# Optimization experiments

Hardware: AMD Instinct MI355X
Metric: run time of the kernel (lower is better)

Reference implementation:

```python
import jax, jax.numpy as jnp
import numpy as np

B, C, L = 64, 128, 1024
SCALES = [8, 4, 2, 1]
EPS_BN = 1e-5


def _ema_vec(x_ds, alpha):
    # x_ds: [B, C, Ls]; alpha: [1, C, 1] in (0,1)
    Ls = x_ds.shape[-1]
    powers = jnp.arange(Ls - 1, -1, -1, dtype=x_ds.dtype)
    base = jnp.power(1.0 - alpha, powers)                                 # [1, C, Ls]
    w_num = jnp.concatenate([base[..., :1], base[..., 1:] * alpha], axis=-1)
    num = jnp.cumsum(x_ds * w_num, axis=-1)
    den = jnp.maximum(jnp.cumsum(base, axis=-1), 1e-12)
    return num / den


def _dwconv(x, w, s):
    # depthwise Conv1d: kernel 2s, stride s, pad s//2, groups=C, no bias
    return jax.lax.conv_general_dilated(
        x, w, window_strides=(s,), padding=[(s // 2, s // 2)],
        dimension_numbers=("NCH", "OIH", "NCH"), feature_group_count=C)


def _proj(v, w1, b1, w2, b2):
    # v: [B, C, Ls] -> Linear(Ls->L), exact GELU, Linear(L->L); torch Linear y = x @ W.T + b
    h = jax.nn.gelu(jnp.einsum("bcs,ls->bcl", v, w1) + b1, approximate=False)
    return jnp.einsum("bcl,ml->bcm", h, w2) + b2


def _hasd(x, bn_g, bn_b, branch, gate):
    Bn = x.shape[0]
    # BatchNorm1d over flattened (C*L) features, training-mode batch stats (biased var)
    v = x.reshape(Bn, C * L)
    mu = v.mean(axis=0)
    var = jnp.mean((v - mu) ** 2, axis=0)
    xn = (((v - mu) / jnp.sqrt(var + EPS_BN)) * bn_g + bn_b).reshape(Bn, C, L)
    trends, seasons, gates = [], [], []
    for s in SCALES:
        if s > 1:
            cw, w1, b1, w2, b2 = branch[s]
            down = _dwconv(xn, cw, s)                                     # [B, C, L//s]
            up = _proj(down, w1, b1, w2, b2)                              # [B, C, L]
        else:
            down = xn
            up = xn
        gw, gb, al = gate[s]
        alpha = jax.nn.sigmoid(al)
        trend_ds = _ema_vec(down, alpha)
        trend_up = _proj(trend_ds, w1, b1, w2, b2) if s > 1 else trend_ds
        season = up - trend_up
        trends.append(trend_up)
        seasons.append(season)
        gates.append(jax.nn.sigmoid(season.mean(axis=-1) @ gw.T + gb))    # [B, 1]
    g = jnp.concatenate(gates, axis=1)                                    # [B, n_scales]
    g = g / (g.sum(axis=1, keepdims=True) + 1e-6)
    g = g[:, :, None, None]
    trend_out = (jnp.stack(trends, axis=1) * g).sum(axis=1)
    season_out = (jnp.stack(seasons, axis=1) * g).sum(axis=1)
    return season_out, trend_out


def setup_inputs() -> dict:
    key = jax.random.key(0)
    ks = iter(jax.random.split(key, 64))
    d = {"x": jax.random.normal(next(ks), (B, C, L), jnp.float32)}
    d["bn_g"] = 1.0 + 0.1 * jax.random.normal(next(ks), (C * L,), jnp.float32)
    d["bn_b"] = 0.1 * jax.random.normal(next(ks), (C * L,), jnp.float32)
    for s in (8, 4, 2):
        Ls = L // s
        d[f"cw{s}"] = jax.random.normal(next(ks), (C, 1, 2 * s), jnp.float32) / np.sqrt(2 * s)
        d[f"w1_{s}"] = jax.random.normal(next(ks), (L, Ls), jnp.float32) / np.sqrt(Ls)
        d[f"b1_{s}"] = jnp.zeros((L,), jnp.float32)
        d[f"w2_{s}"] = jax.random.normal(next(ks), (L, L), jnp.float32) / np.sqrt(L)
        d[f"b2_{s}"] = jnp.zeros((L,), jnp.float32)
    for s in SCALES:
        d[f"gw{s}"] = jax.random.normal(next(ks), (1, C), jnp.float32) / np.sqrt(C)
        d[f"gb{s}"] = jnp.zeros((1,), jnp.float32)
        d[f"al{s}"] = jnp.full((1, C, 1), 0.3, jnp.float32)
    return d


def reference(x, bn_g, bn_b,
              cw8, w1_8, b1_8, w2_8, b2_8,
              cw4, w1_4, b1_4, w2_4, b2_4,
              cw2, w1_2, b1_2, w2_2, b2_2,
              gw8, gb8, al8, gw4, gb4, al4, gw2, gb2, al2, gw1, gb1, al1):
    branch = {8: (cw8, w1_8, b1_8, w2_8, b2_8),
              4: (cw4, w1_4, b1_4, w2_4, b2_4),
              2: (cw2, w1_2, b1_2, w2_2, b2_2)}
    gate = {8: (gw8, gb8, al8), 4: (gw4, gb4, al4),
            2: (gw2, gb2, al2), 1: (gw1, gb1, al1)}
    return _hasd(x, bn_g, bn_b, branch, gate)
```

## Files before the change

kernel.cpp:

```cpp
#include <hip/hip_runtime.h>
#include <hip/hip_bf16.h>
#include <math.h>

#define Bdim 64
#define Cdim 128
#define Ldim 1024
#define BC   (Bdim * Cdim)
#define CLn  (Cdim * Ldim)
#define TOT  (Bdim * CLn)

typedef unsigned short ushort_t;
typedef short s16x8 __attribute__((ext_vector_type(8)));
typedef float f32x4 __attribute__((ext_vector_type(4)));

__device__ __forceinline__ float bf2f(ushort_t u) {
    return __uint_as_float(((unsigned)u) << 16);
}
__device__ __forceinline__ ushort_t f2bf(float f) {
    __hip_bfloat16 h = __float2bfloat16(f);
    return *(ushort_t*)&h;
}
__device__ __forceinline__ void async16(const ushort_t* g, ushort_t* l) {
    __builtin_amdgcn_global_load_lds(
        (const __attribute__((address_space(1))) unsigned int*)g,
        (__attribute__((address_space(3))) unsigned int*)l, 16, 0, 0);
}
__device__ __forceinline__ float fast_gelu(float z) {
    float z2 = z * z;
    float inner = fmaf(0.044715f * z2, z, z);
    float e = __expf(-1.5957691216057308f * inner);
    return z * __builtin_amdgcn_rcpf(1.f + e);
}

__global__ __launch_bounds__(256) void bn_stats_kernel(
    const float* __restrict__ x, const float* __restrict__ bn_g,
    const float* __restrict__ bn_b, float* __restrict__ scale,
    float* __restrict__ shift)
{
    int f = blockIdx.x * 256 + threadIdx.x;
    float sum = 0.f, sumsq = 0.f;
    for (int b = 0; b < Bdim; ++b) {
        float v = x[(size_t)b * CLn + f];
        sum += v; sumsq += v * v;
    }
    float mu  = sum * (1.f / Bdim);
    float var = fmaxf(sumsq * (1.f / Bdim) - mu * mu, 0.f);
    float sc  = bn_g[f] / sqrtf(var + 1e-5f);
    scale[f] = sc;
    shift[f] = bn_b[f] - mu * sc;
}

__global__ __launch_bounds__(256) void convert_weights_kernel(
    const float* __restrict__ w1_8, const float* __restrict__ w1_4,
    const float* __restrict__ w1_2, const float* __restrict__ w2_8,
    const float* __restrict__ w2_4, const float* __restrict__ w2_2,
    ushort_t* __restrict__ dst)
{
    int idx = blockIdx.x * 256 + threadIdx.x;
    const float* src; int off;
    if      (idx < 131072)  { src = w1_8; off = 0; }
    else if (idx < 393216)  { src = w1_4; off = 131072; }
    else if (idx < 917504)  { src = w1_2; off = 393216; }
    else if (idx < 1966080) { src = w2_8; off = 917504; }
    else if (idx < 3014656) { src = w2_4; off = 1966080; }
    else                    { src = w2_2; off = 3014656; }
    dst[idx] = f2bf(src[idx - off]);
}

__global__ __launch_bounds__(256) void w2colsum_kernel(
    const float* __restrict__ w2_8, const float* __restrict__ w2_4,
    const float* __restrict__ w2_2, float* __restrict__ w2cs)
{
    const float* w = (blockIdx.y == 0) ? w2_8 : (blockIdx.y == 1) ? w2_4 : w2_2;
    int h  = blockIdx.x * 64 + (threadIdx.x & 63);
    int ls = threadIdx.x >> 6;
    float s = 0.f;
    for (int l = ls; l < 1024; l += 4) s += w[(size_t)l * 1024 + h];
    __shared__ float red[4][64];
    red[ls][threadIdx.x & 63] = s;
    __syncthreads();
    if (ls == 0)
        w2cs[blockIdx.y * 1024 + h] =
            red[0][threadIdx.x] + red[1][threadIdx.x] +
            red[2][threadIdx.x] + red[3][threadIdx.x];
}

__global__ __launch_bounds__(256) void ema_coef_kernel(
    const float* __restrict__ al1, const float* __restrict__ al2,
    const float* __restrict__ al4, const float* __restrict__ al8,
    float* __restrict__ coef, float* __restrict__ am)
{
    int c   = blockIdx.x;
    int tid = threadIdx.x;
    const float* als[4] = {al1, al2, al4, al8};
    const int Lss[4]    = {1024, 512, 256, 128};
    const int offs[4]   = {0, 1024, 1536, 1792};
#pragma unroll
    for (int si = 0; si < 4; ++si) {
        double a  = 1.0 / (1.0 + exp(-(double)als[si][c]));
        double m  = 1.0 - a;
        double lm = log(m);
        int Ls = Lss[si];
        for (int t = tid; t < Ls; t += 256) {
            double dt  = (1.0 - exp((double)(t + 1) * lm)) / a;
            double den = exp((double)(Ls - 1 - t) * lm) * dt;
            double ramp = (den >= 1e-12) ? 1.0 : den * 1e12;
            coef[(size_t)c * 1920 + offs[si] + t] = (float)(ramp / dt);
        }
        if (tid == 0) {
            am[c * 8 + si * 2 + 0] = (float)a;
            am[c * 8 + si * 2 + 1] = (float)m;
        }
    }
}

template<int SEG>
__device__ __forceinline__ void ema_pass1(
    const float* __restrict__ src, float a, float m, bool lead,
    float* __restrict__ xs, float& Sp, float& Sm)
{
    int lane = threadIdx.x & 63;
    if constexpr (SEG >= 4) {
#pragma unroll
        for (int i = 0; i < SEG; i += 4) {
            f32x4 u = *(const f32x4*)&src[lane * SEG + i];
            xs[i + 0] = u.x; xs[i + 1] = u.y;
            xs[i + 2] = u.z; xs[i + 3] = u.w;
        }
    } else {
        float2 u = *(const float2*)&src[lane * 2];
        xs[0] = u.x; xs[1] = u.y;
    }
    float p = 0.f;
#pragma unroll
    for (int i = 0; i < SEG; ++i) {
        float bi = a * xs[i];
        if (lead && lane == 0 && i == 0) bi = xs[0];
        p = fmaf(m, p, bi);
    }
    float sm = m;
#pragma unroll
    for (int i = 1; i < SEG; ++i) sm *= m;
    Sp = p; Sm = sm;
#pragma unroll
    for (int d = 1; d < 64; d <<= 1) {
        float pm = __shfl_up(Sp, d);
        float mm = __shfl_up(Sm, d);
        if (lane >= d) { Sp = fmaf(Sm, pm, Sp); Sm *= mm; }
    }
}

template<int SEG, bool DIFF>
__device__ __forceinline__ float ema_pass2(
    const float* __restrict__ xs, float a, float m, bool lead, float carry,
    const float* __restrict__ cf, ushort_t* __restrict__ dst)
{
    int lane = threadIdx.x & 63;
    float y = carry, diff = 0.f;
    unsigned pk[(SEG + 1) / 2];
#pragma unroll
    for (int i = 0; i < SEG; ++i) {
        float bi = a * xs[i];
        if (lead && lane == 0 && i == 0) bi = xs[0];
        y = fmaf(m, y, bi);
        float tr = y * cf[lane * SEG + i];
        unsigned h = f2bf(tr);
        if ((i & 1) == 0) pk[i >> 1] = h;
        else              pk[i >> 1] |= h << 16;
        if (DIFF) diff += xs[i] - tr;
    }
    if constexpr (SEG == 8) {
        uint4 v; v.x = pk[0]; v.y = pk[1]; v.z = pk[2]; v.w = pk[3];
        *(uint4*)(dst + lane * 8) = v;
    } else if constexpr (SEG == 4) {
        uint2 v; v.x = pk[0]; v.y = pk[1];
        *(uint2*)(dst + lane * 4) = v;
    } else {
        *(unsigned*)(dst + lane * 2) = pk[0];
    }
    return diff;
}

__global__ __launch_bounds__(256) void pre_kernel(
    const float* __restrict__ x, const float* __restrict__ scale,
    const float* __restrict__ shift,
    const float* __restrict__ cw8, const float* __restrict__ cw4,
    const float* __restrict__ cw2,
    const float* __restrict__ coef, const float* __restrict__ amtab,
    ushort_t* __restrict__ xn_bf, ushort_t* __restrict__ t1_bf,
    ushort_t* __restrict__ A8, ushort_t* __restrict__ A4,
    ushort_t* __restrict__ A2, float* __restrict__ rs)
{
    __shared__ float sxn[1024];
    __shared__ float sxnp[1056];
    __shared__ float sconv[896];
    __shared__ float sP0;
    __shared__ float sdiff[2];
    int r   = blockIdx.x;
    int c   = r & (Cdim - 1);
    int tid = threadIdx.x;

    {
        const float* xr = x + (size_t)r * 1024;
        float4 xv = *(const float4*)(xr + tid * 4);
        float4 sc = *(const float4*)(scale + (size_t)c * 1024 + tid * 4);
        float4 sh = *(const float4*)(shift + (size_t)c * 1024 + tid * 4);
        float v0 = fmaf(xv.x, sc.x, sh.x);
        float v1 = fmaf(xv.y, sc.y, sh.y);
        float v2 = fmaf(xv.z, sc.z, sh.z);
        float v3 = fmaf(xv.w, sc.w, sh.w);
        int p = tid * 4;
        sxn[p + 0] = v0; sxn[p + 1] = v1; sxn[p + 2] = v2; sxn[p + 3] = v3;
        int pp = p + (p >> 5);
        sxnp[pp + 0] = v0; sxnp[pp + 1] = v1;
        sxnp[pp + 2] = v2; sxnp[pp + 3] = v3;
        uint2 pk;
        pk.x = (unsigned)f2bf(v0) | ((unsigned)f2bf(v1) << 16);
        pk.y = (unsigned)f2bf(v2) | ((unsigned)f2bf(v3) << 16);
        *(uint2*)(xn_bf + (size_t)r * 1024 + tid * 4) = pk;
    }
    __syncthreads();

    {
        const float* w2 = cw2 + c * 4;
        unsigned a2pk = 0;
#pragma unroll
        for (int j = 0; j < 2; ++j) {
            int o = tid * 2 + j;
            int start = o * 2 - 1;
            float acc = 0.f;
#pragma unroll
            for (int k = 0; k < 4; ++k) {
                int pos = start + k;
                float v = (pos >= 0 && pos < 1024) ? sxnp[pos + (pos >> 5)] : 0.f;
                acc = fmaf(v, w2[k], acc);
            }
            sconv[o] = acc;
            a2pk |= ((unsigned)f2bf(acc)) << (j * 16);
        }
        *(unsigned*)(A2 + (size_t)r * 512 + tid * 2) = a2pk;
        {
            const float* w4 = cw4 + c * 8;
            int o = tid;
            int start = o * 4 - 2;
            float acc = 0.f;
#pragma unroll
            for (int k = 0; k < 8; ++k) {
                int pos = start + k;
                float v = (pos >= 0 && pos < 1024) ? sxnp[pos + (pos >> 5)] : 0.f;
                acc = fmaf(v, w4[k], acc);
            }
            sconv[512 + o] = acc;
            A4[(size_t)r * 256 + o] = f2bf(acc);
        }
        if (tid < 128) {
            const float* w8 = cw8 + c * 16;
            int o = tid;
            int start = o * 8 - 4;
            float acc = 0.f;
#pragma unroll
            for (int k = 0; k < 16; ++k) {
                int pos = start + k;
                float v = (pos >= 0 && pos < 1024) ? sxnp[pos + (pos >> 5)] : 0.f;
                acc = fmaf(v, w8[k], acc);
            }
            sconv[768 + o] = acc;
            A8[(size_t)r * 128 + o] = f2bf(acc);
        }
    }
    __syncthreads();

    int wave = tid >> 6;
    int lane = tid & 63;
    const float* cf = coef + (size_t)c * 1920;
    const float* am = amtab + c * 8;
    float xs[8];
    float Sp = 0.f, Sm = 1.f, aE = 0.f, mE = 0.f;

    if (wave == 0) {
        aE = am[0]; mE = am[1];
        ema_pass1<8>(sxn, aE, mE, true, xs, Sp, Sm);
        if (lane == 63) sP0 = Sp;
    } else if (wave == 1) {
        aE = am[0]; mE = am[1];
        ema_pass1<8>(sxn + 512, aE, mE, false, xs, Sp, Sm);
    } else if (wave == 2) {
        aE = am[2]; mE = am[3];
        ema_pass1<8>(sconv, aE, mE, true, xs, Sp, Sm);
    } else {
        aE = am[4]; mE = am[5];
        ema_pass1<4>(sconv + 512, aE, mE, true, xs, Sp, Sm);
    }
    __syncthreads();

    float cs  = __shfl_up(Sp, 1);
    float msf = __shfl_up(Sm, 1);
    float carry = lane ? cs : 0.f;

    if (wave == 0) {
        float d = ema_pass2<8, true>(xs, aE, mE, true, carry,
                                     cf, t1_bf + (size_t)r * 1024);
#pragma unroll
        for (int dd = 32; dd; dd >>= 1) d += __shfl_down(d, dd);
        if (lane == 0) sdiff[0] = d;
    } else if (wave == 1) {
        carry += sP0 * (lane ? msf : 1.f);
        float d = ema_pass2<8, true>(xs, aE, mE, false, carry,
                                     cf + 512, t1_bf + (size_t)r * 1024 + 512);
#pragma unroll
        for (int dd = 32; dd; dd >>= 1) d += __shfl_down(d, dd);
        if (lane == 0) sdiff[1] = d;
    } else if (wave == 2) {
        ema_pass2<8, false>(xs, aE, mE, true, carry,
                            cf + 1024, A2 + ((size_t)BC + r) * 512);
    } else {
        ema_pass2<4, false>(xs, aE, mE, true, carry,
                            cf + 1536, A4 + ((size_t)BC + r) * 256);
        float xs2[2];
        aE = am[6]; mE = am[7];
        ema_pass1<2>(sconv + 768, aE, mE, true, xs2, Sp, Sm);
        float cs2 = __shfl_up(Sp, 1);
        float c2  = lane ? cs2 : 0.f;
        ema_pass2<2, false>(xs2, aE, mE, true, c2,
                            cf + 1792, A8 + ((size_t)BC + r) * 128);
    }
    __syncthreads();
    if (tid == 0) rs[3 * BC + r] = sdiff[0] + sdiff[1];
}

__global__ __launch_bounds__(256, 2) void gemm1_kernel(
    const ushort_t* __restrict__ Abase,
    const ushort_t* __restrict__ Wbase,
    const float* __restrict__ b1_8, const float* __restrict__ b1_4,
    const float* __restrict__ b1_2, const float* __restrict__ w2cs,
    ushort_t* __restrict__ Hbase, float* __restrict__ rs)
{
    int gx = blockIdx.x;
    int z  = 2 - (gx >> 6);
    int mi = gx & 63;
    int K = 128 << z;
    const ushort_t* A  = Abase + (size_t)2 * BC * 128 * ((1 << z) - 1);
    const ushort_t* Bw = Wbase + (size_t)131072 * ((1 << z) - 1);
    const float* bias  = (z == 0) ? b1_8 : (z == 1) ? b1_4 : b1_2;
    ushort_t* Hout     = Hbase + (size_t)z * 2 * TOT;

    __shared__ ushort_t Asu[128 * 64];
    __shared__ ushort_t Ast[128 * 64];
    __shared__ ushort_t Bs[128 * 64];
    int tid  = threadIdx.x;
    int wave = tid >> 6;
    int lane = tid & 63;
    int m0 = mi * 128, n0 = blockIdx.y * 128;
    int wm = (wave & 1) * 64, wn = (wave >> 1) * 64;
    int lrow = lane >> 3;
    int pc   = lane & 7;
    int fr   = lane & 15;
    int quad = lane >> 4;

    f32x4 accu[4][4], acct[4][4];
#pragma unroll
    for (int i = 0; i < 4; ++i)
#pragma unroll
        for (int j = 0; j < 4; ++j) {
            accu[i][j] = (f32x4){0.f, 0.f, 0.f, 0.f};
            acct[i][j] = (f32x4){0.f, 0.f, 0.f, 0.f};
        }

    for (int k0 = 0; k0 < K; k0 += 64) {
        __syncthreads();
#pragma unroll
        for (int i = 0; i < 4; ++i) {
            int rb  = wave * 32 + i * 8;
            int row = rb + lrow;
            int lc  = (pc - row) & 7;
            async16(A + (size_t)(m0 + row) * K + k0 + lc * 8,      &Asu[rb * 64]);
            async16(A + (size_t)(BC + m0 + row) * K + k0 + lc * 8, &Ast[rb * 64]);
            async16(Bw + (size_t)(n0 + row) * K + k0 + lc * 8,     &Bs[rb * 64]);
        }
        __syncthreads();
#pragma unroll
        for (int kk = 0; kk < 64; kk += 32) {
            s16x8 af[4], bfr[4];
            int lcA = (kk >> 3) + quad;
#pragma unroll
            for (int t = 0; t < 4; ++t) {
                int nr  = wn + t * 16 + fr;
                bfr[t] = *(const s16x8*)&Bs[nr * 64 + ((lcA + nr) & 7) * 8];
            }
#pragma unroll
            for (int t = 0; t < 4; ++t) {
                int mr  = wm + t * 16 + fr;
                af[t]  = *(const s16x8*)&Asu[mr * 64 + ((lcA + mr) & 7) * 8];
            }
#pragma unroll
            for (int mt = 0; mt < 4; ++mt)
#pragma unroll
                for (int nt = 0; nt < 4; ++nt)
                    accu[mt][nt] = __builtin_amdgcn_mfma_f32_16x16x32_bf16(
                        af[mt], bfr[nt], accu[mt][nt], 0, 0, 0);
#pragma unroll
            for (int t = 0; t < 4; ++t) {
                int mr  = wm + t * 16 + fr;
                af[t]  = *(const s16x8*)&Ast[mr * 64 + ((lcA + mr) & 7) * 8];
            }
#pragma unroll
            for (int mt = 0; mt < 4; ++mt)
#pragma unroll
                for (int nt = 0; nt < 4; ++nt)
                    acct[mt][nt] = __builtin_amdgcn_mfma_f32_16x16x32_bf16(
                        af[mt], bfr[nt], acct[mt][nt], 0, 0, 0);
        }
    }
    float racc[16];
#pragma unroll
    for (int e = 0; e < 16; ++e) racc[e] = 0.f;
#pragma unroll
    for (int mt = 0; mt < 4; ++mt)
#pragma unroll
        for (int nt = 0; nt < 4; ++nt) {
            int col = n0 + wn + nt * 16 + fr;
            float bcol = bias[col];
            float wcs = w2cs[z * 1024 + col];
#pragma unroll
            for (int rr = 0; rr < 4; ++rr) {
                size_t row = m0 + wm + mt * 16 + quad * 4 + rr;
                float gu = fast_gelu(accu[mt][nt][rr] + bcol);
                float gt = fast_gelu(acct[mt][nt][rr] + bcol);
                Hout[row * 1024 + col]        = f2bf(gu);
                Hout[(BC + row) * 1024 + col] = f2bf(gt);
                racc[mt * 4 + rr] = fmaf(gu - gt, wcs, racc[mt * 4 + rr]);
            }
        }
#pragma unroll
    for (int e = 0; e < 16; ++e) {
        float v = racc[e];
        v += __shfl_xor(v, 1); v += __shfl_xor(v, 2);
        v += __shfl_xor(v, 4); v += __shfl_xor(v, 8);
        if (fr == 0) {
            int mt = e >> 2, rr = e & 3;
            int row = m0 + wm + mt * 16 + quad * 4 + rr;
            atomicAdd(&rs[z * BC + row], v);
        }
    }
}

__global__ __launch_bounds__(256, 2) void gemm2_kernel(
    const ushort_t* __restrict__ Hbase,
    const ushort_t* __restrict__ W2base,
    const float* __restrict__ b2_8, const float* __restrict__ b2_4,
    const float* __restrict__ b2_2, const float* __restrict__ g,
    const ushort_t* __restrict__ t1_bf, const ushort_t* __restrict__ xn_bf,
    float* __restrict__ trend_out, float* __restrict__ season_out)
{
    __shared__ ushort_t Asu[128 * 64];
    __shared__ ushort_t Ast[128 * 64];
    __shared__ ushort_t Bs[128 * 64];
    int tid  = threadIdx.x;
    int wave = tid >> 6;
    int lane = tid & 63;
    int m0 = blockIdx.x * 128, n0 = blockIdx.y * 128;
    int wm = (wave & 1) * 64, wn = (wave >> 1) * 64;
    int lrow = lane >> 3;
    int pc   = lane & 7;
    int fr   = lane & 15;
    int quad = lane >> 4;
    int b = m0 >> 7;
    float gv0 = g[b * 4 + 0], gv1 = g[b * 4 + 1], gv2 = g[b * 4 + 2];
    float g1  = g[b * 4 + 3];
    float gsv[3] = {gv0, gv1, gv2};

    f32x4 accu[4][4], acct[4][4];
#pragma unroll
    for (int i = 0; i < 4; ++i)
#pragma unroll
        for (int j = 0; j < 4; ++j) {
            accu[i][j] = (f32x4){0.f, 0.f, 0.f, 0.f};
            acct[i][j] = (f32x4){0.f, 0.f, 0.f, 0.f};
        }

    for (int s = 0; s < 3; ++s) {
        if (s > 0) {
            float rr_ = gsv[s - 1] / fmaxf(gsv[s], 1e-30f);
#pragma unroll
            for (int mt = 0; mt < 4; ++mt)
#pragma unroll
                for (int nt = 0; nt < 4; ++nt)
#pragma unroll
                    for (int rr = 0; rr < 4; ++rr) {
                        accu[mt][nt][rr] *= rr_;
                        acct[mt][nt][rr] *= rr_;
                    }
        }
        const ushort_t* Au = Hbase + (size_t)s * 2 * TOT;
        const ushort_t* At = Au + TOT;
        const ushort_t* Bw = W2base + (size_t)s * 1048576;
        for (int k0 = 0; k0 < 1024; k0 += 64) {
            __syncthreads();
#pragma unroll
            for (int i = 0; i < 4; ++i) {
                int rb  = wave * 32 + i * 8;
                int row = rb + lrow;
                int lc  = (pc - row) & 7;
                async16(Au + (size_t)(m0 + row) * 1024 + k0 + lc * 8, &Asu[rb * 64]);
                async16(At + (size_t)(m0 + row) * 1024 + k0 + lc * 8, &Ast[rb * 64]);
                async16(Bw + (size_t)(n0 + row) * 1024 + k0 + lc * 8, &Bs[rb * 64]);
            }
            __syncthreads();
#pragma unroll
            for (int kk = 0; kk < 64; kk += 32) {
                s16x8 af[4], bfr[4];
                int lcA = (kk >> 3) + quad;
#pragma unroll
                for (int t = 0; t < 4; ++t) {
                    int nr  = wn + t * 16 + fr;
                    bfr[t] = *(const s16x8*)&Bs[nr * 64 + ((lcA + nr) & 7) * 8];
                }
#pragma unroll
                for (int t = 0; t < 4; ++t) {
                    int mr  = wm + t * 16 + fr;
                    af[t]  = *(const s16x8*)&Asu[mr * 64 + ((lcA + mr) & 7) * 8];
                }
#pragma unroll
                for (int mt = 0; mt < 4; ++mt)
#pragma unroll
                    for (int nt = 0; nt < 4; ++nt)
                        accu[mt][nt] = __builtin_amdgcn_mfma_f32_16x16x32_bf16(
                            af[mt], bfr[nt], accu[mt][nt], 0, 0, 0);
#pragma unroll
                for (int t = 0; t < 4; ++t) {
                    int mr  = wm + t * 16 + fr;
                    af[t]  = *(const s16x8*)&Ast[mr * 64 + ((lcA + mr) & 7) * 8];
                }
#pragma unroll
                for (int mt = 0; mt < 4; ++mt)
#pragma unroll
                    for (int nt = 0; nt < 4; ++nt)
                        acct[mt][nt] = __builtin_amdgcn_mfma_f32_16x16x32_bf16(
                            af[mt], bfr[nt], acct[mt][nt], 0, 0, 0);
            }
        }
    }
#pragma unroll
    for (int mt = 0; mt < 4; ++mt)
#pragma unroll
        for (int nt = 0; nt < 4; ++nt)
#pragma unroll
            for (int rr = 0; rr < 4; ++rr) {
                accu[mt][nt][rr] *= gv2;
                acct[mt][nt][rr] *= gv2;
            }

#pragma unroll
    for (int mt = 0; mt < 4; ++mt)
#pragma unroll
        for (int nt = 0; nt < 4; ++nt) {
            int col = n0 + wn + nt * 16 + fr;
            float cb2 = gv0 * b2_8[col] + gv1 * b2_4[col] + gv2 * b2_2[col];
#pragma unroll
            for (int r = 0; r < 4; ++r) {
                size_t row = m0 + wm + mt * 16 + quad * 4 + r;
                size_t idx = row * 1024 + col;
                float tr = acct[mt][nt][r] + cb2 + g1 * bf2f(t1_bf[idx]);
                float se = accu[mt][nt][r] + cb2 + g1 * bf2f(xn_bf[idx]) - tr;
                trend_out[idx]  = tr;
                season_out[idx] = se;
            }
        }
}

__global__ __launch_bounds__(128) void gate_kernel(
    const float* __restrict__ rs,
    const float* __restrict__ gw8, const float* __restrict__ gb8,
    const float* __restrict__ gw4, const float* __restrict__ gb4,
    const float* __restrict__ gw2, const float* __restrict__ gb2,
    const float* __restrict__ gw1, const float* __restrict__ gb1,
    float* __restrict__ g)
{
    int b = blockIdx.x;
    int c = threadIdx.x;
    const float* gws[4] = {gw8, gw4, gw2, gw1};
    const float* gbs[4] = {gb8, gb4, gb2, gb1};
    __shared__ float buf[128];
    __shared__ float gates[4];
    for (int si = 0; si < 4; ++si) {
        buf[c] = rs[si * BC + b * Cdim + c] * (1.f / Ldim) * gws[si][c];
        __syncthreads();
        for (int off = 64; off >= 1; off >>= 1) {
            if (c < off) buf[c] += buf[c + off];
            __syncthreads();
        }
        if (c == 0) {
            float z = buf[0] + gbs[si][0];
            gates[si] = 1.f / (1.f + expf(-z));
        }
        __syncthreads();
    }
    if (c == 0) {
        float s = gates[0] + gates[1] + gates[2] + gates[3] + 1e-6f;
#pragma unroll
        for (int si = 0; si < 4; ++si) g[b * 4 + si] = gates[si] / s;
    }
}

extern "C" void kernel_launch(void* const* d_in, const int* in_sizes, int n_in,
                              void* d_out, int out_size, void* d_ws, size_t ws_size,
                              hipStream_t stream)
{
    const float* x    = (const float*)d_in[0];
    const float* bn_g = (const float*)d_in[1];
    const float* bn_b = (const float*)d_in[2];
    const float* cw8  = (const float*)d_in[3];
    const float* w1_8 = (const float*)d_in[4];
    const float* b1_8 = (const float*)d_in[5];
    const float* w2_8 = (const float*)d_in[6];
    const float* b2_8 = (const float*)d_in[7];
    const float* cw4  = (const float*)d_in[8];
    const float* w1_4 = (const float*)d_in[9];
    const float* b1_4 = (const float*)d_in[10];
    const float* w2_4 = (const float*)d_in[11];
    const float* b2_4 = (const float*)d_in[12];
    const float* cw2  = (const float*)d_in[13];
    const float* w1_2 = (const float*)d_in[14];
    const float* b1_2 = (const float*)d_in[15];
    const float* w2_2 = (const float*)d_in[16];
    const float* b2_2 = (const float*)d_in[17];
    const float* gw8  = (const float*)d_in[18];
    const float* gb8  = (const float*)d_in[19];
    const float* al8  = (const float*)d_in[20];
    const float* gw4  = (const float*)d_in[21];
    const float* gb4  = (const float*)d_in[22];
    const float* al4  = (const float*)d_in[23];
    const float* gw2  = (const float*)d_in[24];
    const float* gb2  = (const float*)d_in[25];
    const float* al2  = (const float*)d_in[26];
    const float* gw1  = (const float*)d_in[27];
    const float* gb1  = (const float*)d_in[28];
    const float* al1  = (const float*)d_in[29];

    ushort_t* p_xn  = (ushort_t*)d_ws;
    ushort_t* p_t1  = p_xn + TOT;
    ushort_t* p_H   = p_t1 + TOT;
    ushort_t* p_wb  = p_H + 6 * (size_t)TOT;
    ushort_t* p_w1b = p_wb;
    ushort_t* p_w2b = p_wb + 917504;
    float*    p_sc  = (float*)(p_wb + 4063232);
    float*    p_sh  = p_sc + CLn;
    float*    p_w2cs = p_sh + CLn;
    float*    p_rs  = p_w2cs + 3 * 1024;
    float*    p_g   = p_rs + 4 * BC;
    float*    p_coef = (float*)p_H;
    float*    p_am   = p_coef + 128 * 1920;
    ushort_t* p_A8 = (ushort_t*)d_out;
    ushort_t* p_A4 = p_A8 + 2 * (size_t)BC * 128;
    ushort_t* p_A2 = p_A4 + 2 * (size_t)BC * 256;
    float*    p_season = (float*)d_out;
    float*    p_trend  = (float*)d_out + TOT;

    hipMemsetAsync(p_rs, 0, 4 * BC * sizeof(float), stream);
    bn_stats_kernel<<<CLn / 256, 256, 0, stream>>>(x, bn_g, bn_b, p_sc, p_sh);
    ema_coef_kernel<<<128, 256, 0, stream>>>(al1, al2, al4, al8, p_coef, p_am);
    convert_weights_kernel<<<4063232 / 256, 256, 0, stream>>>(
        w1_8, w1_4, w1_2, w2_8, w2_4, w2_2, p_wb);
    w2colsum_kernel<<<dim3(16, 3), 256, 0, stream>>>(w2_8, w2_4, w2_2, p_w2cs);

    pre_kernel<<<BC, 256, 0, stream>>>(x, p_sc, p_sh, cw8, cw4, cw2,
                                       p_coef, p_am,
                                       p_xn, p_t1, p_A8, p_A4, p_A2, p_rs);

    gemm1_kernel<<<dim3(192, 8), 256, 0, stream>>>(
        p_A8, p_w1b, b1_8, b1_4, b1_2, p_w2cs, p_H, p_rs);

    gate_kernel<<<Bdim, 128, 0, stream>>>(p_rs, gw8, gb8, gw4, gb4,
                                          gw2, gb2, gw1, gb1, p_g);

    gemm2_kernel<<<dim3(64, 8), 256, 0, stream>>>(
        p_H, p_w2b, b2_8, b2_4, b2_2, p_g, p_t1, p_xn, p_trend, p_season);
}
```

Baseline: 426.1 us.

## Double-buffer GEMM K-tiles with async LDS prefetch in both GEMM kernels

Both GEMM kernels move from a single-buffered 64-wide K loop to a double-buffered 32-wide K loop. The next tile is prefetched with global_load_lds while the current one is computed, using explicit vmcnt waits and raw barriers, with a new 4-way swizzle. gemm2 folds its three scale passes into one flat 96-step pipeline so prefetching continues across scale boundaries. MFMA sections run at raised wave priority. LDS use per block stays the same, but each tile now needs two barriers and the per-step K chunk is halved, which adds synchronization overhead.

```diff
diff --git a/kernel.cpp b/kernel.cpp
--- a/kernel.cpp
+++ b/kernel.cpp
@@ -335,25 +335,24 @@
     const float* __restrict__ b1_2, const float* __restrict__ w2cs,
     ushort_t* __restrict__ Hbase, float* __restrict__ rs)
 {
+    __shared__ ushort_t smem[24576];
     int gx = blockIdx.x;
     int z  = 2 - (gx >> 6);
     int mi = gx & 63;
-    int K = 128 << z;
+    int K  = 128 << z;
+    int NT = K >> 5;
     const ushort_t* A  = Abase + (size_t)2 * BC * 128 * ((1 << z) - 1);
     const ushort_t* Bw = Wbase + (size_t)131072 * ((1 << z) - 1);
     const float* bias  = (z == 0) ? b1_8 : (z == 1) ? b1_4 : b1_2;
     ushort_t* Hout     = Hbase + (size_t)z * 2 * TOT;
 
-    __shared__ ushort_t Asu[128 * 64];
-    __shared__ ushort_t Ast[128 * 64];
-    __shared__ ushort_t Bs[128 * 64];
     int tid  = threadIdx.x;
     int wave = tid >> 6;
     int lane = tid & 63;
     int m0 = mi * 128, n0 = blockIdx.y * 128;
     int wm = (wave & 1) * 64, wn = (wave >> 1) * 64;
-    int lrow = lane >> 3;
-    int pc   = lane & 7;
+    int rlow = lane >> 2;
+    int s4   = lane & 3;
     int fr   = lane & 15;
     int quad = lane >> 4;
 
@@ -366,51 +365,62 @@
             acct[i][j] = (f32x4){0.f, 0.f, 0.f, 0.f};
         }
 
-    for (int k0 = 0; k0 < K; k0 += 64) {
-        __syncthreads();
-#pragma unroll
-        for (int i = 0; i < 4; ++i) {
-            int rb  = wave * 32 + i * 8;
-            int row = rb + lrow;
-            int lc  = (pc - row) & 7;
-            async16(A + (size_t)(m0 + row) * K + k0 + lc * 8,      &Asu[rb * 64]);
-            async16(A + (size_t)(BC + m0 + row) * K + k0 + lc * 8, &Ast[rb * 64]);
-            async16(Bw + (size_t)(n0 + row) * K + k0 + lc * 8,     &Bs[rb * 64]);
-        }
-        __syncthreads();
-#pragma unroll
-        for (int kk = 0; kk < 64; kk += 32) {
-            s16x8 af[4], bfr[4];
-            int lcA = (kk >> 3) + quad;
-#pragma unroll
-            for (int t = 0; t < 4; ++t) {
-                int nr  = wn + t * 16 + fr;
-                bfr[t] = *(const s16x8*)&Bs[nr * 64 + ((lcA + nr) & 7) * 8];
-            }
-#pragma unroll
-            for (int t = 0; t < 4; ++t) {
-                int mr  = wm + t * 16 + fr;
-                af[t]  = *(const s16x8*)&Asu[mr * 64 + ((lcA + mr) & 7) * 8];
-            }
-#pragma unroll
-            for (int mt = 0; mt < 4; ++mt)
-#pragma unroll
-                for (int nt = 0; nt < 4; ++nt)
-                    accu[mt][nt] = __builtin_amdgcn_mfma_f32_16x16x32_bf16(
-                        af[mt], bfr[nt], accu[mt][nt], 0, 0, 0);
-#pragma unroll
-            for (int t = 0; t < 4; ++t) {
-                int mr  = wm + t * 16 + fr;
-                af[t]  = *(const s16x8*)&Ast[mr * 64 + ((lcA + mr) & 7) * 8];
-            }
-#pragma unroll
-            for (int mt = 0; mt < 4; ++mt)
-#pragma unroll
-                for (int nt = 0; nt < 4; ++nt)
-                    acct[mt][nt] = __builtin_amdgcn_mfma_f32_16x16x32_bf16(
-                        af[mt], bfr[nt], acct[mt][nt], 0, 0, 0);
-        }
-    }
+    auto stage = [&](int t, int buf) {
+        int k0 = t * 32;
+        ushort_t* base = smem + buf * 12288;
+#pragma unroll
+        for (int i = 0; i < 2; ++i) {
+            int rb  = wave * 32 + i * 16;
+            int row = rb + rlow;
+            int cg  = (s4 - (row >> 1)) & 3;
+            async16(A  + (size_t)(m0 + row) * K + k0 + cg * 8,      base + rb * 32);
+            async16(A  + (size_t)(BC + m0 + row) * K + k0 + cg * 8, base + 4096 + rb * 32);
+            async16(Bw + (size_t)(n0 + row) * K + k0 + cg * 8,      base + 8192 + rb * 32);
+        }
+    };
+
+    stage(0, 0);
+    int cur = 0;
+    for (int t = 0; t < NT; ++t) {
+        if (t + 1 < NT) {
+            stage(t + 1, cur ^ 1);
+            asm volatile("s_waitcnt vmcnt(6)" ::: "memory");
+        } else {
+            asm volatile("s_waitcnt vmcnt(0)" ::: "memory");
+        }
+        __builtin_amdgcn_s_barrier();
+        __builtin_amdgcn_sched_barrier(0);
+        const ushort_t* Au_ = smem + cur * 12288;
+        const ushort_t* At_ = Au_ + 4096;
+        const ushort_t* Bs_ = Au_ + 8192;
+        s16x8 afu[4], aft[4], bfr[4];
+#pragma unroll
+        for (int q = 0; q < 4; ++q) {
+            int nr = wn + q * 16 + fr;
+            bfr[q] = *(const s16x8*)&Bs_[nr * 32 + ((quad + (nr >> 1)) & 3) * 8];
+            int mr = wm + q * 16 + fr;
+            afu[q] = *(const s16x8*)&Au_[mr * 32 + ((quad + (mr >> 1)) & 3) * 8];
+            aft[q] = *(const s16x8*)&At_[mr * 32 + ((quad + (mr >> 1)) & 3) * 8];
+        }
+        __builtin_amdgcn_s_setprio(1);
+#pragma unroll
+        for (int mt = 0; mt < 4; ++mt)
+#pragma unroll
+            for (int nt = 0; nt < 4; ++nt)
+                accu[mt][nt] = __builtin_amdgcn_mfma_f32_16x16x32_bf16(
+                    afu[mt], bfr[nt], accu[mt][nt], 0, 0, 0);
+#pragma unroll
+        for (int mt = 0; mt < 4; ++mt)
+#pragma unroll
+            for (int nt = 0; nt < 4; ++nt)
+                acct[mt][nt] = __builtin_amdgcn_mfma_f32_16x16x32_bf16(
+                    aft[mt], bfr[nt], acct[mt][nt], 0, 0, 0);
+        __builtin_amdgcn_s_setprio(0);
+        __builtin_amdgcn_sched_barrier(0);
+        __builtin_amdgcn_s_barrier();
+        cur ^= 1;
+    }
+
     float racc[16];
 #pragma unroll
     for (int e = 0; e < 16; ++e) racc[e] = 0.f;
@@ -452,16 +462,14 @@
     const ushort_t* __restrict__ t1_bf, const ushort_t* __restrict__ xn_bf,
     float* __restrict__ trend_out, float* __restrict__ season_out)
 {
-    __shared__ ushort_t Asu[128 * 64];
-    __shared__ ushort_t Ast[128 * 64];
-    __shared__ ushort_t Bs[128 * 64];
+    __shared__ ushort_t smem[24576];
     int tid  = threadIdx.x;
     int wave = tid >> 6;
     int lane = tid & 63;
     int m0 = blockIdx.x * 128, n0 = blockIdx.y * 128;
     int wm = (wave & 1) * 64, wn = (wave >> 1) * 64;
-    int lrow = lane >> 3;
-    int pc   = lane & 7;
+    int rlow = lane >> 2;
+    int s4   = lane & 3;
     int fr   = lane & 15;
     int quad = lane >> 4;
     int b = m0 >> 7;
@@ -478,8 +486,39 @@
             acct[i][j] = (f32x4){0.f, 0.f, 0.f, 0.f};
         }
 
-    for (int s = 0; s < 3; ++s) {
-        if (s > 0) {
+    auto stage = [&](int kt, int buf) {
+        int s  = kt >> 5;
+        int k0 = (kt & 31) * 32;
+        const ushort_t* Au = Hbase + (size_t)s * 2 * TOT;
+        const ushort_t* At = Au + TOT;
+        const ushort_t* Bw = W2base + (size_t)s * 1048576;
+        ushort_t* base = smem + buf * 12288;
+#pragma unroll
+        for (int i = 0; i < 2; ++i) {
+            int rb  = wave * 32 + i * 16;
+            int row = rb + rlow;
+            int cg  = (s4 - (row >> 1)) & 3;
+            size_t goff = (size_t)(m0 + row) * 1024 + k0 + cg * 8;
+            async16(Au + goff, base + rb * 32);
+            async16(At + goff, base + 4096 + rb * 32);
+            async16(Bw + (size_t)(n0 + row) * 1024 + k0 + cg * 8,
+                    base + 8192 + rb * 32);
+        }
+    };
+
+    stage(0, 0);
+    int cur = 0;
+    for (int kt = 0; kt < 96; ++kt) {
+        if (kt + 1 < 96) {
+            stage(kt + 1, cur ^ 1);
+            asm volatile("s_waitcnt vmcnt(6)" ::: "memory");
+        } else {
+            asm volatile("s_waitcnt vmcnt(0)" ::: "memory");
+        }
+        __builtin_amdgcn_s_barrier();
+        __builtin_amdgcn_sched_barrier(0);
+        if (kt > 0 && (kt & 31) == 0) {
+            int s = kt >> 5;
             float rr_ = gsv[s - 1] / fmaxf(gsv[s], 1e-30f);
 #pragma unroll
             for (int mt = 0; mt < 4; ++mt)
@@ -491,54 +530,35 @@
                         acct[mt][nt][rr] *= rr_;
                     }
         }
-        const ushort_t* Au = Hbase + (size_t)s * 2 * TOT;
-        const ushort_t* At = Au + TOT;
-        const ushort_t* Bw = W2base + (size_t)s * 1048576;
-        for (int k0 = 0; k0 < 1024; k0 += 64) {
-            __syncthreads();
-#pragma unroll
-            for (int i = 0; i < 4; ++i) {
-                int rb  = wave * 32 + i * 8;
-                int row = rb + lrow;
-                int lc  = (pc - row) & 7;
-                async16(Au + (size_t)(m0 + row) * 1024 + k0 + lc * 8, &Asu[rb * 64]);
-                async16(At + (size_t)(m0 + row) * 1024 + k0 + lc * 8, &Ast[rb * 64]);
-                async16(Bw + (size_t)(n0 + row) * 1024 + k0 + lc * 8, &Bs[rb * 64]);
-            }
-            __syncthreads();
-#pragma unroll
-            for (int kk = 0; kk < 64; kk += 32) {
-                s16x8 af[4], bfr[4];
-                int lcA = (kk >> 3) + quad;
-#pragma unroll
-                for (int t = 0; t < 4; ++t) {
-                    int nr  = wn + t * 16 + fr;
-                    bfr[t] = *(const s16x8*)&Bs[nr * 64 + ((lcA + nr) & 7) * 8];
-                }
-#pragma unroll
-                for (int t = 0; t < 4; ++t) {
-                    int mr  = wm + t * 16 + fr;
-                    af[t]  = *(const s16x8*)&Asu[mr * 64 + ((lcA + mr) & 7) * 8];
-                }
-#pragma unroll
-                for (int mt = 0; mt < 4; ++mt)
-#pragma unroll
-                    for (int nt = 0; nt < 4; ++nt)
-                        accu[mt][nt] = __builtin_amdgcn_mfma_f32_16x16x32_bf16(
-                            af[mt], bfr[nt], accu[mt][nt], 0, 0, 0);
-#pragma unroll
-                for (int t = 0; t < 4; ++t) {
-                    int mr  = wm + t * 16 + fr;
-                    af[t]  = *(const s16x8*)&Ast[mr * 64 + ((lcA + mr) & 7) * 8];
-                }
-#pragma unroll
-                for (int mt = 0; mt < 4; ++mt)
-#pragma unroll
-                    for (int nt = 0; nt < 4; ++nt)
-                        acct[mt][nt] = __builtin_amdgcn_mfma_f32_16x16x32_bf16(
-                            af[mt], bfr[nt], acct[mt][nt], 0, 0, 0);
-            }
-        }
+        const ushort_t* Au_ = smem + cur * 12288;
+        const ushort_t* At_ = Au_ + 4096;
+        const ushort_t* Bs_ = Au_ + 8192;
+        s16x8 afu[4], aft[4], bfr[4];
+#pragma unroll
+        for (int q = 0; q < 4; ++q) {
+            int nr = wn + q * 16 + fr;
+            bfr[q] = *(const s16x8*)&Bs_[nr * 32 + ((quad + (nr >> 1)) & 3) * 8];
+            int mr = wm + q * 16 + fr;
+            afu[q] = *(const s16x8*)&Au_[mr * 32 + ((quad + (mr >> 1)) & 3) * 8];
+            aft[q] = *(const s16x8*)&At_[mr * 32 + ((quad + (mr >> 1)) & 3) * 8];
+        }
+        __builtin_amdgcn_s_setprio(1);
+#pragma unroll
+        for (int mt = 0; mt < 4; ++mt)
+#pragma unroll
+            for (int nt = 0; nt < 4; ++nt)
+                accu[mt][nt] = __builtin_amdgcn_mfma_f32_16x16x32_bf16(
+                    afu[mt], bfr[nt], accu[mt][nt], 0, 0, 0);
+#pragma unroll
+        for (int mt = 0; mt < 4; ++mt)
+#pragma unroll
+            for (int nt = 0; nt < 4; ++nt)
+                acct[mt][nt] = __builtin_amdgcn_mfma_f32_16x16x32_bf16(
+                    aft[mt], bfr[nt], acct[mt][nt], 0, 0, 0);
+        __builtin_amdgcn_s_setprio(0);
+        __builtin_amdgcn_sched_barrier(0);
+        __builtin_amdgcn_s_barrier();
+        cur ^= 1;
     }
 #pragma unroll
     for (int mt = 0; mt < 4; ++mt)
```

New measurement: 434.5 us. No clear change (+2.0%).
